# Kernel tuning notes

Hardware: AMD Instinct MI355X
Metric: run time of the kernel (lower is better)

Reference implementation:

```python
import jax, jax.numpy as jnp
import numpy as np

N = 4096        # number of nodes
C = 512         # in_features
L_LAT = 64      # L_latent
EPS = 0.25      # epsilon


def setup_inputs() -> dict:
    key = jax.random.key(0)
    ks = jax.random.split(key, 8)
    def lin(k, fan_in, shape):
        return (jax.random.normal(k, shape, jnp.float32) / np.float32(np.sqrt(fan_in)))
    x = jax.random.normal(ks[0], (N, C), jnp.float32)
    adj = jax.random.uniform(ks[1], (N, N), jnp.float32)  # dense nonneg kernel
    W_proj = lin(ks[2], C, (C, L_LAT)); b_proj = jnp.zeros((L_LAT,), jnp.float32)
    W_pi1 = lin(ks[3], L_LAT, (L_LAT, C)); b_pi1 = jnp.zeros((C,), jnp.float32)
    W_pi2 = lin(ks[4], C, (C, 1)); b_pi2 = jnp.zeros((1,), jnp.float32)
    W_f = lin(ks[5], C, (C, C)); b_f = jnp.zeros((C,), jnp.float32)
    dt = jnp.array([0.1], jnp.float32)
    return {"x": x, "adj": adj, "W_proj": W_proj, "b_proj": b_proj,
            "W_pi1": W_pi1, "b_pi1": b_pi1, "W_pi2": W_pi2, "b_pi2": b_pi2,
            "W_f": W_f, "b_f": b_f, "dt": dt}


def reference(x, adj, W_proj, b_proj, W_pi1, b_pi1, W_pi2, b_pi2, W_f, b_f, dt):
    # proj_list: x -> latent [n, L]
    z = x @ W_proj + b_proj
    # pi_list: Linear -> ReLU -> Linear -> Sigmoid, squeeze to [n]
    pi = jax.nn.sigmoid(jax.nn.relu(z @ W_pi1 + b_pi1) @ W_pi2 + b_pi2)[:, 0]
    # q_epsilon_tilde: row sums of the kernel
    q = adj.sum(axis=1)                       # [n]
    # K_tilde = K_epsilon @ diag(pi/q)  == column scaling
    K_tilde = adj * (pi / q)[None, :]         # [n, n]
    # D_tilde diagonal; torch.inverse of a diagonal == elementwise reciprocal
    d = K_tilde.sum(axis=1) + 1e-5            # [n]
    # target = relu(f(x)) with f = Linear(C, C)
    target = jax.nn.relu(x @ W_f + b_f)       # [n, C]
    # L @ target = (1/eps) * diag(1/d) @ K_tilde @ target - target
    Lt = (K_tilde @ target) / (EPS * d)[:, None] - target
    return target + dt[0] * Lt
```

## Files before the change

kernel.cpp:

```cpp
#include <hip/hip_runtime.h>
#include <hip/hip_bf16.h>

#define N_NODES 4096
#define C_DIM   512
#define L_DIM   64
#define SPLITS  4
#define KCHUNK  (N_NODES / SPLITS)

typedef unsigned short u16;
typedef unsigned int   u32;
using bf16x8 = __attribute__((ext_vector_type(8))) __bf16;
using u16x8  = __attribute__((ext_vector_type(8))) unsigned short;
using f32x4  = __attribute__((ext_vector_type(4))) float;

__device__ __forceinline__ float b2f(u16 u) {
    union { unsigned int i; float f; } v; v.i = ((unsigned int)u) << 16; return v.f;
}
__device__ __forceinline__ u16 f2b(float f) {
    __bf16 h = (__bf16)f;
    union { __bf16 h; u16 u; } v; v.h = h; return v.u;
}
__device__ __forceinline__ void gload16(const void* g, void* l) {
    __builtin_amdgcn_global_load_lds((const __attribute__((address_space(1))) void*)g,
                                     (__attribute__((address_space(3))) void*)l,
                                     16, 0, 0);
}
__device__ __forceinline__ int detect_mode_inl(const u16* __restrict__ adj) {
    int m = 0;
#pragma unroll
    for (int i = 0; i < 64; ++i) m |= (adj[i] >= 0x8000) ? 1 : 0;
    return m;
}
__device__ __forceinline__ float ldin(const void* p, int i, int mode) {
    if (mode) return ((const float*)p)[i];
    return b2f(((const u16*)p)[i]);
}

#define OFF_MODE  0
#define OFF_DT    64
#define OFF_BIAS  1024
#define OFF_BP    4096
#define OFF_BP1   4608
#define OFF_WP2   8192
#define OFF_BP2   10240
#define OFF_Q     16384
#define OFF_S     32768
#define OFF_DV    49152
#define OFF_WPP   65536
#define OFF_WP1P  131072
#define OFF_WFT   196608
#define OFF_PACC  720896
#define OFF_TST   9437184
#define OFF_XB    13631488
#define OFF_ADJB  17825792

__global__ __launch_bounds__(256) void k1_prep(const void* __restrict__ adj, const void* __restrict__ x,
        const void* Wp, const void* bp, const void* Wp1, const void* bp1,
        const void* Wp2, const void* bp2, const void* Wf, const void* bfc, const void* dt,
        int* __restrict__ modep,
        float* __restrict__ bp_f, float* __restrict__ bp1_f,
        float* __restrict__ Wp2_f, float* __restrict__ bp2_f,
        float* __restrict__ bias_f, float* __restrict__ dt_f,
        u32* __restrict__ WpP, u32* __restrict__ Wp1P,
        u16* __restrict__ adjb, float* __restrict__ q, u16* __restrict__ xb,
        u16* __restrict__ WfT, float* __restrict__ Pacc2, float* __restrict__ dvraw) {
    __shared__ float tile[32][33];
    int bid = blockIdx.x, tid = threadIdx.x;
    int mode = detect_mode_inl((const u16*)adj);
    if (bid < 1024) {
        int wave = tid >> 6, lane = tid & 63;
        int row = bid * 4 + wave;
        float acc = 0.f;
        if (mode) {
            const float4* rp = (const float4*)((const float*)adj + (size_t)row * N_NODES);
            ushort4* wp = (ushort4*)(adjb + (size_t)row * N_NODES);
#pragma unroll 8
            for (int it = 0; it < 16; ++it) {
                float4 v = rp[it * 64 + lane];
                acc += (v.x + v.y) + (v.z + v.w);
                ushort4 o; o.x = f2b(v.x); o.y = f2b(v.y); o.z = f2b(v.z); o.w = f2b(v.w);
                wp[it * 64 + lane] = o;
            }
        } else {
            const u16x8* rp = (const u16x8*)((const u16*)adj + (size_t)row * N_NODES);
#pragma unroll
            for (int it = 0; it < 8; ++it) {
                u16x8 v = rp[it * 64 + lane];
#pragma unroll
                for (int e = 0; e < 8; ++e) acc += b2f(v[e]);
            }
        }
#pragma unroll
        for (int off = 32; off > 0; off >>= 1) acc += __shfl_down(acc, off);
        if (lane == 0) q[row] = acc;
    } else if (bid < 3072) {
        if (mode == 0) return;
        int idx = (bid - 1024) * 256 + tid;
        float4 v = ((const float4*)x)[idx];
        ushort4 o; o.x = f2b(v.x); o.y = f2b(v.y); o.z = f2b(v.z); o.w = f2b(v.w);
        ((ushort4*)xb)[idx] = o;
    } else if (bid < 3328) {
        int g = bid - 3072;
        int tx = tid & 31, ty = tid >> 5;
        int x0 = (g & 15) * 32, y0 = (g >> 4) * 32;
        if (mode) {
            const float* src = (const float*)Wf;
#pragma unroll
            for (int r = ty; r < 32; r += 8) tile[r][tx] = src[(size_t)(y0 + r) * C_DIM + x0 + tx];
        } else {
            const u16* src = (const u16*)Wf;
#pragma unroll
            for (int r = ty; r < 32; r += 8) tile[r][tx] = b2f(src[(size_t)(y0 + r) * C_DIM + x0 + tx]);
        }
        __syncthreads();
#pragma unroll
        for (int r = ty; r < 32; r += 8)
            WfT[(size_t)(x0 + r) * C_DIM + y0 + tx] = f2b(tile[tx][r]);
    } else if (bid < 3392) {
        int idx = (bid - 3328) * 256 + tid;
        int k2i = idx >> 6, j = idx & 63;
        float a = ldin(Wp, (2 * k2i) * L_DIM + j, mode);
        float b = ldin(Wp, (2 * k2i + 1) * L_DIM + j, mode);
        WpP[idx] = (u32)f2b(a) | ((u32)f2b(b) << 16);
    } else if (bid < 3456) {
        int idx = (bid - 3392) * 256 + tid;
        int jj2 = idx >> 9, m = idx & 511;
        float a = ldin(Wp1, (2 * jj2) * C_DIM + m, mode);
        float b = ldin(Wp1, (2 * jj2 + 1) * C_DIM + m, mode);
        Wp1P[idx] = (u32)f2b(a) | ((u32)f2b(b) << 16);
    } else if (bid < 3463) {
        if (bid == 3456 && tid == 0) *modep = mode;
        int idx = (bid - 3456) * 256 + tid;
        if (idx < 64)           bp_f[idx]          = ldin(bp,  idx, mode);
        else if (idx < 576)     bp1_f[idx - 64]    = ldin(bp1, idx - 64, mode);
        else if (idx < 1088)    Wp2_f[idx - 576]   = ldin(Wp2, idx - 576, mode);
        else if (idx == 1088)   bp2_f[0]           = ldin(bp2, 0, mode);
        else if (idx < 1601)    bias_f[idx - 1089] = ldin(bfc, idx - 1089, mode);
        else if (idx == 1601)   dt_f[0]            = ldin(dt, 0, mode);
    } else if (bid < 5511) {
        int idx = (bid - 3463) * 256 + tid;
        ((float4*)Pacc2)[idx] = make_float4(0.f, 0.f, 0.f, 0.f);
    } else {
        int idx = (bid - 5511) * 256 + tid;
        dvraw[idx] = 0.f;
    }
}

__global__ __launch_bounds__(256) void k1p_pi(const void* __restrict__ xraw,
        const int* __restrict__ modep, const u16* __restrict__ xb,
        const u32* __restrict__ WpP, const u32* __restrict__ Wp1P,
        const float* __restrict__ bp_f,  const float* __restrict__ bp1_f,
        const float* __restrict__ Wp2_f, const float* __restrict__ bp2_f,
        const float* __restrict__ q, float* __restrict__ s) {
    __shared__ __align__(16) char smem[26880];
    int bid = blockIdx.x, tid = threadIdx.x;
    int mode = *modep;
    float (*sx)[C_DIM]      = (float(*)[C_DIM])smem;
    float (*red)[8][L_DIM]  = (float(*)[8][L_DIM])(smem + 16384);
    float (*sz)[L_DIM]      = (float(*)[L_DIM])(smem + 24576);
    float (*rw)[8]          = (float(*)[8])(smem + 26624);
    int i0 = bid * 8;
    const u16* xsrc = mode ? xb : (const u16*)xraw;
    const u16x8* xp = (const u16x8*)(xsrc + (size_t)i0 * C_DIM);
#pragma unroll
    for (int r = 0; r < 2; ++r) {
        u16x8 v = xp[tid + 256 * r];
        float* dstf = &sx[0][0] + (size_t)(tid + 256 * r) * 8;
#pragma unroll
        for (int e = 0; e < 8; ++e) dstf[e] = b2f(v[e]);
    }
    __syncthreads();
    int j = tid & 63, part = tid >> 6;
    float za[8];
#pragma unroll
    for (int n = 0; n < 8; ++n) za[n] = 0.f;
    const u32* wp = WpP + part * 4096 + j;
#pragma unroll 8
    for (int kk = 0; kk < 64; ++kk) {
        u32 w = wp[kk * 64];
        float wa = b2f((u16)(w & 0xFFFF)), wb = b2f((u16)(w >> 16));
        int k = part * 128 + kk * 2;
#pragma unroll
        for (int n = 0; n < 8; ++n) za[n] += sx[n][k] * wa + sx[n][k + 1] * wb;
    }
#pragma unroll
    for (int n = 0; n < 8; ++n) red[part][n][j] = za[n];
    __syncthreads();
#pragma unroll
    for (int r = 0; r < 2; ++r) {
        int idx = tid + r * 256; int n = idx >> 6, jj = idx & 63;
        sz[n][jj] = red[0][n][jj] + red[1][n][jj] + red[2][n][jj] + red[3][n][jj] + bp_f[jj];
    }
    __syncthreads();
    int m0 = tid, m1 = tid + 256;
    float h0[8], h1[8];
    float b0 = bp1_f[m0], b1 = bp1_f[m1];
#pragma unroll
    for (int n = 0; n < 8; ++n) { h0[n] = b0; h1[n] = b1; }
    const u32* w1p = Wp1P + m0;
#pragma unroll 4
    for (int jj2 = 0; jj2 < 32; ++jj2) {
        u32 w0 = w1p[jj2 * 512], w1 = w1p[jj2 * 512 + 256];
        float w0a = b2f((u16)(w0 & 0xFFFF)), w0b = b2f((u16)(w0 >> 16));
        float w1a = b2f((u16)(w1 & 0xFFFF)), w1b = b2f((u16)(w1 >> 16));
#pragma unroll
        for (int n = 0; n < 8; ++n) {
            float za_ = sz[n][2 * jj2], zb_ = sz[n][2 * jj2 + 1];
            h0[n] += za_ * w0a + zb_ * w0b;
            h1[n] += za_ * w1a + zb_ * w1b;
        }
    }
    float w2a = Wp2_f[m0], w2b = Wp2_f[m1];
    float p[8];
#pragma unroll
    for (int n = 0; n < 8; ++n)
        p[n] = fmaxf(h0[n], 0.f) * w2a + fmaxf(h1[n], 0.f) * w2b;
#pragma unroll
    for (int off = 32; off > 0; off >>= 1)
#pragma unroll
        for (int n = 0; n < 8; ++n) p[n] += __shfl_down(p[n], off);
    int lane = tid & 63, wave = tid >> 6;
    if (lane == 0) {
#pragma unroll
        for (int n = 0; n < 8; ++n) rw[wave][n] = p[n];
    }
    __syncthreads();
    if (tid < 8) {
        float tot = rw[0][tid] + rw[1][tid] + rw[2][tid] + rw[3][tid] + bp2_f[0];
        float pi = 1.f / (1.f + expf(-tot));
        s[i0 + tid] = pi / q[i0 + tid];
    }
}

__global__ __launch_bounds__(256) void k2_gemm1(const void* __restrict__ xraw,
        const int* __restrict__ modep,
        const float* __restrict__ s, const float* __restrict__ bias_f, const float* __restrict__ dt_f,
        const u16* __restrict__ xb, const u16* __restrict__ WfT,
        u16* __restrict__ TsT, void* __restrict__ out, float* __restrict__ Pacc_base) {
    __shared__ __align__(16) char smem[16640];
    int bid = blockIdx.x, tid = threadIdx.x;
    int mode = *modep;
    u16* lA = (u16*)smem;
    u16* lB = (u16*)(smem + 8192);
    u16* lT = (u16*)smem;
    float* s_row = (float*)(smem + 16384);
    int lane = tid & 63, wave = tid >> 6;
    int bm = (bid & 63) * 64, bn = (bid >> 6) * 64;
    if (tid < 64) s_row[tid] = s[bm + tid];
    const u16* Axb = mode ? xb : (const u16*)xraw;
    float* basep = mode ? (float*)out : Pacc_base;
    int quad = lane >> 4, l15 = lane & 15;
    int wm = wave * 16;
    int trow = tid >> 3;
    int xslot = (tid & 7) ^ (trow & 7);
    const u16* Ap0 = Axb + (size_t)(bm + trow) * C_DIM + xslot * 8;
    const u16* Ap1 = Axb + (size_t)(bm + 32 + trow) * C_DIM + xslot * 8;
    const u16* Bp0 = WfT + (size_t)(bn + trow) * C_DIM + xslot * 8;
    const u16* Bp1 = WfT + (size_t)(bn + 32 + trow) * C_DIM + xslot * 8;
    f32x4 acc[4];
#pragma unroll
    for (int nt = 0; nt < 4; ++nt) acc[nt] = (f32x4){0.f, 0.f, 0.f, 0.f};
    for (int k0 = 0; k0 < C_DIM; k0 += 64) {
        gload16(Ap0 + k0, lA + tid * 8);
        gload16(Ap1 + k0, lA + 2048 + tid * 8);
        gload16(Bp0 + k0, lB + tid * 8);
        gload16(Bp1 + k0, lB + 2048 + tid * 8);
        asm volatile("s_waitcnt vmcnt(0)\n\ts_barrier" ::: "memory");
        __builtin_amdgcn_sched_barrier(0);
#pragma unroll
        for (int kk = 0; kk < 2; ++kk) {
            int xr = (((kk << 2) | quad) ^ (l15 & 7)) * 8;
            bf16x8 af = *(const bf16x8*)&lA[(wm + l15) * 64 + xr];
            bf16x8 bfv[4];
#pragma unroll
            for (int nt = 0; nt < 4; ++nt)
                bfv[nt] = *(const bf16x8*)&lB[(nt * 16 + l15) * 64 + xr];
#pragma unroll
            for (int nt = 0; nt < 4; ++nt)
                acc[nt] = __builtin_amdgcn_mfma_f32_16x16x32_bf16(af, bfv[nt], acc[nt], 0, 0, 0);
        }
        asm volatile("s_waitcnt lgkmcnt(0)\n\ts_barrier" ::: "memory");
    }
    float c0 = 1.f - dt_f[0];
#pragma unroll
    for (int nt = 0; nt < 4; ++nt) {
        int col_l = nt * 16 + l15;
        float bv = bias_f[bn + col_l];
#pragma unroll
        for (int r = 0; r < 4; ++r) {
            int row_l = wm + quad * 4 + r;
            float t = fmaxf(acc[nt][r] + bv, 0.f);
            basep[(size_t)(bm + row_l) * C_DIM + bn + col_l] = c0 * t;
            lT[col_l * 64 + row_l] = f2b(t * s_row[row_l]);
        }
    }
    __syncthreads();
    int col_l = tid >> 2, seg = tid & 3;
    uint4 w0 = *(const uint4*)&lT[col_l * 64 + seg * 16];
    uint4 w1 = *(const uint4*)&lT[col_l * 64 + seg * 16 + 8];
    u16* dst = TsT + (size_t)(bn + col_l) * N_NODES + bm + seg * 16;
    *(uint4*)dst = w0;
    *(uint4*)(dst + 8) = w1;
}

__global__ __launch_bounds__(256) void k3_gemm2(const void* __restrict__ adjraw,
        const int* __restrict__ modep,
        const u16* __restrict__ adjb, const u16* __restrict__ TsT,
        const float* __restrict__ s,
        float* __restrict__ Pacc2, float* __restrict__ dvraw) {
    __shared__ __align__(16) u16 lA[8192];
    __shared__ __align__(16) u16 lB[8192];
    int mode = *modep;
    const u16* A = mode ? adjb : (const u16*)adjraw;
    int tid = threadIdx.x;
    int id = blockIdx.x;
    int xcd = id & 7, local = id >> 3;
    if (local < 64) {
        int lane = tid & 63, wave = tid >> 6;
        int bm128 = (xcd * 4 + (local >> 4)) * 128;
        int bn128 = ((local >> 2) & 3) * 128;
        int kbase = (local & 3) * KCHUNK;
        int wm = (wave & 1) * 64, wn = (wave >> 1) * 64;
        int quad = lane >> 4, l15 = lane & 15;
        int trow = tid >> 3;
        int xslot = (tid & 7) ^ (trow & 7);

        const u16* Ap[4]; const u16* Bp[4];
#pragma unroll
        for (int i = 0; i < 4; ++i) {
            Ap[i] = A   + (size_t)(bm128 + i * 32 + trow) * N_NODES + kbase + xslot * 8;
            Bp[i] = TsT + (size_t)(bn128 + i * 32 + trow) * N_NODES + kbase + xslot * 8;
        }

        f32x4 acc[4][4];
#pragma unroll
        for (int a = 0; a < 4; ++a)
#pragma unroll
            for (int b = 0; b < 4; ++b) acc[a][b] = (f32x4){0.f, 0.f, 0.f, 0.f};

        for (int k0 = 0; k0 < KCHUNK; k0 += 64) {
#pragma unroll
            for (int i = 0; i < 4; ++i) gload16(Ap[i] + k0, lA + i * 2048 + tid * 8);
#pragma unroll
            for (int i = 0; i < 4; ++i) gload16(Bp[i] + k0, lB + i * 2048 + tid * 8);
            asm volatile("s_waitcnt vmcnt(0)\n\ts_barrier" ::: "memory");
            __builtin_amdgcn_sched_barrier(0);
#pragma unroll
            for (int kk = 0; kk < 2; ++kk) {
                int xr = (((kk << 2) | quad) ^ (l15 & 7)) * 8;
                bf16x8 af[4], bfv[4];
#pragma unroll
                for (int mt = 0; mt < 4; ++mt) af[mt] = *(const bf16x8*)&lA[(wm + mt * 16 + l15) * 64 + xr];
#pragma unroll
                for (int nt = 0; nt < 4; ++nt) bfv[nt] = *(const bf16x8*)&lB[(wn + nt * 16 + l15) * 64 + xr];
#pragma unroll
                for (int mt = 0; mt < 4; ++mt)
#pragma unroll
                    for (int nt = 0; nt < 4; ++nt)
                        acc[mt][nt] = __builtin_amdgcn_mfma_f32_16x16x32_bf16(af[mt], bfv[nt], acc[mt][nt], 0, 0, 0);
            }
            asm volatile("s_waitcnt lgkmcnt(0)\n\ts_barrier" ::: "memory");
        }

#pragma unroll
        for (int mt = 0; mt < 4; ++mt) {
#pragma unroll
            for (int nt = 0; nt < 4; ++nt) {
                int col = bn128 + wn + nt * 16 + l15;
#pragma unroll
                for (int r = 0; r < 4; ++r) {
                    int row = bm128 + wm + mt * 16 + quad * 4 + r;
                    atomicAdd(&Pacc2[(size_t)row * C_DIM + col], acc[mt][nt][r]);
                }
            }
        }
    } else {
        int l2 = local - 64;
        int bm128 = (xcd * 4 + (l2 >> 2)) * 128;
        int kbase = (l2 & 3) * KCHUNK;
        float* s_lds = (float*)lA;
        ((float4*)s_lds)[tid] = ((const float4*)(s + kbase))[tid];
        __syncthreads();
        int lane = tid & 63, wave = tid >> 6;
        const u16* base_row = A + (size_t)(bm128 + wave * 32) * N_NODES + kbase;
        for (int r = 0; r < 32; ++r) {
            const u16x8* rp = (const u16x8*)(base_row + (size_t)r * N_NODES) + lane;
            float acc = 0.f;
#pragma unroll
            for (int it = 0; it < 2; ++it) {
                u16x8 v = rp[it * 64];
                const float* sp = s_lds + it * 512 + lane * 8;
#pragma unroll
                for (int e = 0; e < 8; ++e) acc += b2f(v[e]) * sp[e];
            }
#pragma unroll
            for (int off = 32; off > 0; off >>= 1) acc += __shfl_down(acc, off);
            if (lane == 0) atomicAdd(&dvraw[bm128 + wave * 32 + r], acc);
        }
    }
}

__global__ __launch_bounds__(256) void k5_fin(const int* __restrict__ modep,
                                              const float* __restrict__ dt_f,
                                              const float* __restrict__ Pacc2,
                                              const float* __restrict__ dvraw,
                                              const float* __restrict__ Pacc_base,
                                              void* __restrict__ out) {
    int mode = *modep;
    int idx = blockIdx.x * 256 + threadIdx.x;
    float c1 = dt_f[0] * 4.f;
    const float4* basep = mode ? (const float4*)out : (const float4*)Pacc_base;
    float4 b = basep[idx];
    float4 p = ((const float4*)Pacc2)[idx];
    int row = idx >> 7;
    float rscale = c1 / (dvraw[row] + 1e-5f);
    float4 v;
    v.x = b.x + p.x * rscale;
    v.y = b.y + p.y * rscale;
    v.z = b.z + p.z * rscale;
    v.w = b.w + p.w * rscale;
    if (mode) {
        ((float4*)out)[idx] = v;
    } else {
        ushort4 o; o.x = f2b(v.x); o.y = f2b(v.y); o.z = f2b(v.z); o.w = f2b(v.w);
        ((ushort4*)out)[idx] = o;
    }
}

extern "C" void kernel_launch(void* const* d_in, const int* in_sizes, int n_in,
                              void* d_out, int out_size, void* d_ws, size_t ws_size,
                              hipStream_t stream) {
    const void* x   = d_in[0];
    const void* adj = d_in[1];
    const void* Wp  = d_in[2];
    const void* bp  = d_in[3];
    const void* Wp1 = d_in[4];
    const void* bp1 = d_in[5];
    const void* Wp2 = d_in[6];
    const void* bp2 = d_in[7];
    const void* Wf  = d_in[8];
    const void* bfc = d_in[9];
    const void* dtp = d_in[10];

    char* ws = (char*)d_ws;
    int*   modep  = (int*)(ws + OFF_MODE);
    float* dt_f   = (float*)(ws + OFF_DT);
    float* bias_f = (float*)(ws + OFF_BIAS);
    float* bp_f   = (float*)(ws + OFF_BP);
    float* bp1_f  = (float*)(ws + OFF_BP1);
    float* Wp2_f  = (float*)(ws + OFF_WP2);
    float* bp2_f  = (float*)(ws + OFF_BP2);
    float* q      = (float*)(ws + OFF_Q);
    float* s      = (float*)(ws + OFF_S);
    float* dvraw  = (float*)(ws + OFF_DV);
    u32*   WpP    = (u32*)(ws + OFF_WPP);
    u32*   Wp1P   = (u32*)(ws + OFF_WP1P);
    u16*   WfT    = (u16*)(ws + OFF_WFT);
    float* Pacc2  = (float*)(ws + OFF_PACC);
    u16*   TsT    = (u16*)(ws + OFF_TST);
    u16*   xb     = (u16*)(ws + OFF_XB);
    u16*   adjb   = (u16*)(ws + OFF_ADJB);
    float* Pacc_base = (float*)(ws + OFF_ADJB);

    k1_prep<<<5527, 256, 0, stream>>>(adj, x, Wp, bp, Wp1, bp1, Wp2, bp2, Wf, bfc, dtp,
                                      modep, bp_f, bp1_f, Wp2_f, bp2_f, bias_f, dt_f,
                                      WpP, Wp1P, adjb, q, xb, WfT, Pacc2, dvraw);
    k1p_pi<<<512, 256, 0, stream>>>(x, modep, xb, WpP, Wp1P, bp_f, bp1_f, Wp2_f, bp2_f, q, s);
    k2_gemm1<<<512, 256, 0, stream>>>(x, modep, s, bias_f, dt_f, xb, WfT, TsT, d_out, Pacc_base);
    k3_gemm2<<<640, 256, 0, stream>>>(adj, modep, adjb, TsT, s, Pacc2, dvraw);
    k5_fin<<<2048, 256, 0, stream>>>(modep, dt_f, Pacc2, dvraw, Pacc_base, d_out);
}
```

Before: 234.5 us.

## Fuse d-vector matvec into GEMM2 via MFMA, memset accumulators, coarsen prep/fin

The separate d = adj·s row-reduction blocks in the second GEMM are replaced by an extra MFMA per k-step, issued from blockIdx.y==0 waves, with s staged in LDS and masked into one B column. The grid becomes a 3D launch without XCD remapping, and the LDS layout drops the XOR swizzle in favor of two 32-wide k halves. Zeroing the accumulators moves from prep blocks to hipMemsetAsync, and the prep and finish kernels process several elements per thread. The explicit waitcnt/barrier asm is replaced by __syncthreads. Risks include LDS bank conflicts from the unswizzled layout, lost XCD locality, and extra MFMA work on some waves.

```diff
diff --git a/kernel.cpp b/kernel.cpp
--- a/kernel.cpp
+++ b/kernel.cpp
@@ -63,7 +63,7 @@
         float* __restrict__ bias_f, float* __restrict__ dt_f,
         u32* __restrict__ WpP, u32* __restrict__ Wp1P,
         u16* __restrict__ adjb, float* __restrict__ q, u16* __restrict__ xb,
-        u16* __restrict__ WfT, float* __restrict__ Pacc2, float* __restrict__ dvraw) {
+        u16* __restrict__ WfT) {
     __shared__ float tile[32][33];
     int bid = blockIdx.x, tid = threadIdx.x;
     int mode = detect_mode_inl((const u16*)adj);
@@ -93,14 +93,18 @@
 #pragma unroll
         for (int off = 32; off > 0; off >>= 1) acc += __shfl_down(acc, off);
         if (lane == 0) q[row] = acc;
-    } else if (bid < 3072) {
+    } else if (bid < 1152) {
         if (mode == 0) return;
-        int idx = (bid - 1024) * 256 + tid;
-        float4 v = ((const float4*)x)[idx];
-        ushort4 o; o.x = f2b(v.x); o.y = f2b(v.y); o.z = f2b(v.z); o.w = f2b(v.w);
-        ((ushort4*)xb)[idx] = o;
-    } else if (bid < 3328) {
-        int g = bid - 3072;
+        int base = (bid - 1024) * 256 + tid;
+#pragma unroll
+        for (int i = 0; i < 16; ++i) {
+            int idx = i * 32768 + base;
+            float4 v = ((const float4*)x)[idx];
+            ushort4 o; o.x = f2b(v.x); o.y = f2b(v.y); o.z = f2b(v.z); o.w = f2b(v.w);
+            ((ushort4*)xb)[idx] = o;
+        }
+    } else if (bid < 1408) {
+        int g = bid - 1152;
         int tx = tid & 31, ty = tid >> 5;
         int x0 = (g & 15) * 32, y0 = (g >> 4) * 32;
         if (mode) {
@@ -116,33 +120,35 @@
 #pragma unroll
         for (int r = ty; r < 32; r += 8)
             WfT[(size_t)(x0 + r) * C_DIM + y0 + tx] = f2b(tile[tx][r]);
-    } else if (bid < 3392) {
-        int idx = (bid - 3328) * 256 + tid;
-        int k2i = idx >> 6, j = idx & 63;
-        float a = ldin(Wp, (2 * k2i) * L_DIM + j, mode);
-        float b = ldin(Wp, (2 * k2i + 1) * L_DIM + j, mode);
-        WpP[idx] = (u32)f2b(a) | ((u32)f2b(b) << 16);
-    } else if (bid < 3456) {
-        int idx = (bid - 3392) * 256 + tid;
-        int jj2 = idx >> 9, m = idx & 511;
-        float a = ldin(Wp1, (2 * jj2) * C_DIM + m, mode);
-        float b = ldin(Wp1, (2 * jj2 + 1) * C_DIM + m, mode);
-        Wp1P[idx] = (u32)f2b(a) | ((u32)f2b(b) << 16);
-    } else if (bid < 3463) {
-        if (bid == 3456 && tid == 0) *modep = mode;
-        int idx = (bid - 3456) * 256 + tid;
+    } else if (bid < 1416) {
+        int base = (bid - 1408) * 2048 + tid;
+#pragma unroll
+        for (int i = 0; i < 8; ++i) {
+            int idx = base + i * 256;
+            int k2i = idx >> 6, j = idx & 63;
+            float a = ldin(Wp, (2 * k2i) * L_DIM + j, mode);
+            float b = ldin(Wp, (2 * k2i + 1) * L_DIM + j, mode);
+            WpP[idx] = (u32)f2b(a) | ((u32)f2b(b) << 16);
+        }
+    } else if (bid < 1424) {
+        int base = (bid - 1416) * 2048 + tid;
+#pragma unroll
+        for (int i = 0; i < 8; ++i) {
+            int idx = base + i * 256;
+            int jj2 = idx >> 9, m = idx & 511;
+            float a = ldin(Wp1, (2 * jj2) * C_DIM + m, mode);
+            float b = ldin(Wp1, (2 * jj2 + 1) * C_DIM + m, mode);
+            Wp1P[idx] = (u32)f2b(a) | ((u32)f2b(b) << 16);
+        }
+    } else {
+        if (bid == 1424 && tid == 0) *modep = mode;
+        int idx = (bid - 1424) * 256 + tid;
         if (idx < 64)           bp_f[idx]          = ldin(bp,  idx, mode);
         else if (idx < 576)     bp1_f[idx - 64]    = ldin(bp1, idx - 64, mode);
         else if (idx < 1088)    Wp2_f[idx - 576]   = ldin(Wp2, idx - 576, mode);
         else if (idx == 1088)   bp2_f[0]           = ldin(bp2, 0, mode);
         else if (idx < 1601)    bias_f[idx - 1089] = ldin(bfc, idx - 1089, mode);
         else if (idx == 1601)   dt_f[0]            = ldin(dt, 0, mode);
-    } else if (bid < 5511) {
-        int idx = (bid - 3463) * 256 + tid;
-        ((float4*)Pacc2)[idx] = make_float4(0.f, 0.f, 0.f, 0.f);
-    } else {
-        int idx = (bid - 5511) * 256 + tid;
-        dvraw[idx] = 0.f;
     }
 }
 
@@ -265,8 +271,7 @@
         gload16(Ap1 + k0, lA + 2048 + tid * 8);
         gload16(Bp0 + k0, lB + tid * 8);
         gload16(Bp1 + k0, lB + 2048 + tid * 8);
-        asm volatile("s_waitcnt vmcnt(0)\n\ts_barrier" ::: "memory");
-        __builtin_amdgcn_sched_barrier(0);
+        __syncthreads();
 #pragma unroll
         for (int kk = 0; kk < 2; ++kk) {
             int xr = (((kk << 2) | quad) ^ (l15 & 7)) * 8;
@@ -279,7 +284,7 @@
             for (int nt = 0; nt < 4; ++nt)
                 acc[nt] = __builtin_amdgcn_mfma_f32_16x16x32_bf16(af, bfv[nt], acc[nt], 0, 0, 0);
         }
-        asm volatile("s_waitcnt lgkmcnt(0)\n\ts_barrier" ::: "memory");
+        __syncthreads();
     }
     float c0 = 1.f - dt_f[0];
 #pragma unroll
@@ -310,93 +315,97 @@
         float* __restrict__ Pacc2, float* __restrict__ dvraw) {
     __shared__ __align__(16) u16 lA[8192];
     __shared__ __align__(16) u16 lB[8192];
+    __shared__ __align__(16) u16 s_s[1024];
     int mode = *modep;
     const u16* A = mode ? adjb : (const u16*)adjraw;
     int tid = threadIdx.x;
-    int id = blockIdx.x;
-    int xcd = id & 7, local = id >> 3;
-    if (local < 64) {
-        int lane = tid & 63, wave = tid >> 6;
-        int bm128 = (xcd * 4 + (local >> 4)) * 128;
-        int bn128 = ((local >> 2) & 3) * 128;
-        int kbase = (local & 3) * KCHUNK;
-        int wm = (wave & 1) * 64, wn = (wave >> 1) * 64;
-        int quad = lane >> 4, l15 = lane & 15;
-        int trow = tid >> 3;
-        int xslot = (tid & 7) ^ (trow & 7);
-
-        const u16* Ap[4]; const u16* Bp[4];
-#pragma unroll
-        for (int i = 0; i < 4; ++i) {
-            Ap[i] = A   + (size_t)(bm128 + i * 32 + trow) * N_NODES + kbase + xslot * 8;
-            Bp[i] = TsT + (size_t)(bn128 + i * 32 + trow) * N_NODES + kbase + xslot * 8;
-        }
-
-        f32x4 acc[4][4];
-#pragma unroll
-        for (int a = 0; a < 4; ++a)
-#pragma unroll
-            for (int b = 0; b < 4; ++b) acc[a][b] = (f32x4){0.f, 0.f, 0.f, 0.f};
-
-        for (int k0 = 0; k0 < KCHUNK; k0 += 64) {
-#pragma unroll
-            for (int i = 0; i < 4; ++i) gload16(Ap[i] + k0, lA + i * 2048 + tid * 8);
-#pragma unroll
-            for (int i = 0; i < 4; ++i) gload16(Bp[i] + k0, lB + i * 2048 + tid * 8);
-            asm volatile("s_waitcnt vmcnt(0)\n\ts_barrier" ::: "memory");
-            __builtin_amdgcn_sched_barrier(0);
-#pragma unroll
-            for (int kk = 0; kk < 2; ++kk) {
-                int xr = (((kk << 2) | quad) ^ (l15 & 7)) * 8;
-                bf16x8 af[4], bfv[4];
-#pragma unroll
-                for (int mt = 0; mt < 4; ++mt) af[mt] = *(const bf16x8*)&lA[(wm + mt * 16 + l15) * 64 + xr];
-#pragma unroll
-                for (int nt = 0; nt < 4; ++nt) bfv[nt] = *(const bf16x8*)&lB[(wn + nt * 16 + l15) * 64 + xr];
+    int lane = tid & 63, wave = tid >> 6;
+    int bm = blockIdx.x * 128, bn = blockIdx.y * 128;
+    int kbase = blockIdx.z * KCHUNK;
+    int wm = (wave & 1) * 64, wn = (wave >> 1) * 64;
+    int quad = lane >> 4, l15 = lane & 15;
+    bool do_d = (blockIdx.y == 0) && (wave < 2);
+
+#pragma unroll
+    for (int i = 0; i < 4; ++i) {
+        int k = tid + i * 256;
+        s_s[k] = f2b(s[kbase + k]);
+    }
+
+    const u16* Ab0 = A + (size_t)(bm + (tid >> 2)) * N_NODES + kbase + (tid & 3) * 8;
+    const u16* Ab1 = A + (size_t)(bm + 64 + (tid >> 2)) * N_NODES + kbase + (tid & 3) * 8;
+    const u16* Bb0 = TsT + (size_t)(bn + (tid >> 2)) * N_NODES + kbase + (tid & 3) * 8;
+    const u16* Bb1 = TsT + (size_t)(bn + 64 + (tid >> 2)) * N_NODES + kbase + (tid & 3) * 8;
+    u16* la00 = lA + tid * 8;        u16* la01 = lA + 2048 + tid * 8;
+    u16* la10 = lA + 4096 + tid * 8; u16* la11 = lA + 6144 + tid * 8;
+    u16* lb00 = lB + tid * 8;        u16* lb01 = lB + 2048 + tid * 8;
+    u16* lb10 = lB + 4096 + tid * 8; u16* lb11 = lB + 6144 + tid * 8;
+
+    f32x4 acc[4][4];
+#pragma unroll
+    for (int a = 0; a < 4; ++a)
+#pragma unroll
+        for (int b = 0; b < 4; ++b) acc[a][b] = (f32x4){0.f, 0.f, 0.f, 0.f};
+    f32x4 accd[4];
+#pragma unroll
+    for (int a = 0; a < 4; ++a) accd[a] = (f32x4){0.f, 0.f, 0.f, 0.f};
+    u16 dmask = (l15 == 0) ? (u16)0xFFFFu : (u16)0;
+
+    for (int k0 = 0; k0 < KCHUNK; k0 += 64) {
+        gload16(Ab0 + k0, la00);
+        gload16(Ab1 + k0, la01);
+        gload16(Ab0 + k0 + 32, la10);
+        gload16(Ab1 + k0 + 32, la11);
+        gload16(Bb0 + k0, lb00);
+        gload16(Bb1 + k0, lb01);
+        gload16(Bb0 + k0 + 32, lb10);
+        gload16(Bb1 + k0 + 32, lb11);
+        __syncthreads();
+#pragma unroll
+        for (int kk = 0; kk < 2; ++kk) {
+            const u16* baseA = lA + kk * 4096;
+            const u16* baseB = lB + kk * 4096;
+            bf16x8 af[4], bfv[4];
+#pragma unroll
+            for (int mt = 0; mt < 4; ++mt) af[mt] = *(const bf16x8*)&baseA[(wm + mt * 16 + l15) * 32 + quad * 8];
+#pragma unroll
+            for (int nt = 0; nt < 4; ++nt) bfv[nt] = *(const bf16x8*)&baseB[(wn + nt * 16 + l15) * 32 + quad * 8];
+#pragma unroll
+            for (int mt = 0; mt < 4; ++mt)
+#pragma unroll
+                for (int nt = 0; nt < 4; ++nt)
+                    acc[mt][nt] = __builtin_amdgcn_mfma_f32_16x16x32_bf16(af[mt], bfv[nt], acc[mt][nt], 0, 0, 0);
+            if (do_d) {
+                u16x8 su = *(const u16x8*)&s_s[k0 + kk * 32 + quad * 8];
+#pragma unroll
+                for (int e = 0; e < 8; ++e) su[e] &= dmask;
+                bf16x8 bs = *(bf16x8*)&su;
 #pragma unroll
                 for (int mt = 0; mt < 4; ++mt)
-#pragma unroll
-                    for (int nt = 0; nt < 4; ++nt)
-                        acc[mt][nt] = __builtin_amdgcn_mfma_f32_16x16x32_bf16(af[mt], bfv[nt], acc[mt][nt], 0, 0, 0);
+                    accd[mt] = __builtin_amdgcn_mfma_f32_16x16x32_bf16(af[mt], bs, accd[mt], 0, 0, 0);
             }
-            asm volatile("s_waitcnt lgkmcnt(0)\n\ts_barrier" ::: "memory");
-        }
-
-#pragma unroll
-        for (int mt = 0; mt < 4; ++mt) {
-#pragma unroll
-            for (int nt = 0; nt < 4; ++nt) {
-                int col = bn128 + wn + nt * 16 + l15;
-#pragma unroll
-                for (int r = 0; r < 4; ++r) {
-                    int row = bm128 + wm + mt * 16 + quad * 4 + r;
-                    atomicAdd(&Pacc2[(size_t)row * C_DIM + col], acc[mt][nt][r]);
-                }
+        }
+        __syncthreads();
+    }
+
+#pragma unroll
+    for (int mt = 0; mt < 4; ++mt) {
+#pragma unroll
+        for (int nt = 0; nt < 4; ++nt) {
+            int col = bn + wn + nt * 16 + l15;
+#pragma unroll
+            for (int r = 0; r < 4; ++r) {
+                int row = bm + wm + mt * 16 + quad * 4 + r;
+                atomicAdd(&Pacc2[(size_t)row * C_DIM + col], acc[mt][nt][r]);
             }
         }
-    } else {
-        int l2 = local - 64;
-        int bm128 = (xcd * 4 + (l2 >> 2)) * 128;
-        int kbase = (l2 & 3) * KCHUNK;
-        float* s_lds = (float*)lA;
-        ((float4*)s_lds)[tid] = ((const float4*)(s + kbase))[tid];
-        __syncthreads();
-        int lane = tid & 63, wave = tid >> 6;
-        const u16* base_row = A + (size_t)(bm128 + wave * 32) * N_NODES + kbase;
-        for (int r = 0; r < 32; ++r) {
-            const u16x8* rp = (const u16x8*)(base_row + (size_t)r * N_NODES) + lane;
-            float acc = 0.f;
-#pragma unroll
-            for (int it = 0; it < 2; ++it) {
-                u16x8 v = rp[it * 64];
-                const float* sp = s_lds + it * 512 + lane * 8;
-#pragma unroll
-                for (int e = 0; e < 8; ++e) acc += b2f(v[e]) * sp[e];
-            }
-#pragma unroll
-            for (int off = 32; off > 0; off >>= 1) acc += __shfl_down(acc, off);
-            if (lane == 0) atomicAdd(&dvraw[bm128 + wave * 32 + r], acc);
-        }
+    }
+    if (do_d && l15 == 0) {
+#pragma unroll
+        for (int mt = 0; mt < 4; ++mt)
+#pragma unroll
+            for (int r = 0; r < 4; ++r)
+                atomicAdd(&dvraw[bm + wm + mt * 16 + quad * 4 + r], accd[mt][r]);
     }
 }
 
@@ -407,23 +416,26 @@
                                               const float* __restrict__ Pacc_base,
                                               void* __restrict__ out) {
     int mode = *modep;
-    int idx = blockIdx.x * 256 + threadIdx.x;
     float c1 = dt_f[0] * 4.f;
     const float4* basep = mode ? (const float4*)out : (const float4*)Pacc_base;
-    float4 b = basep[idx];
-    float4 p = ((const float4*)Pacc2)[idx];
-    int row = idx >> 7;
-    float rscale = c1 / (dvraw[row] + 1e-5f);
-    float4 v;
-    v.x = b.x + p.x * rscale;
-    v.y = b.y + p.y * rscale;
-    v.z = b.z + p.z * rscale;
-    v.w = b.w + p.w * rscale;
-    if (mode) {
-        ((float4*)out)[idx] = v;
-    } else {
-        ushort4 o; o.x = f2b(v.x); o.y = f2b(v.y); o.z = f2b(v.z); o.w = f2b(v.w);
-        ((ushort4*)out)[idx] = o;
+#pragma unroll
+    for (int i = 0; i < 8; ++i) {
+        int idx = blockIdx.x * 2048 + i * 256 + threadIdx.x;
+        float4 b = basep[idx];
+        float4 p = ((const float4*)Pacc2)[idx];
+        int row = idx >> 7;
+        float rscale = c1 / (dvraw[row] + 1e-5f);
+        float4 v;
+        v.x = b.x + p.x * rscale;
+        v.y = b.y + p.y * rscale;
+        v.z = b.z + p.z * rscale;
+        v.w = b.w + p.w * rscale;
+        if (mode) {
+            ((float4*)out)[idx] = v;
+        } else {
+            ushort4 o; o.x = f2b(v.x); o.y = f2b(v.y); o.z = f2b(v.z); o.w = f2b(v.w);
+            ((ushort4*)out)[idx] = o;
+        }
     }
 }
 
@@ -462,11 +474,13 @@
     u16*   adjb   = (u16*)(ws + OFF_ADJB);
     float* Pacc_base = (float*)(ws + OFF_ADJB);
 
-    k1_prep<<<5527, 256, 0, stream>>>(adj, x, Wp, bp, Wp1, bp1, Wp2, bp2, Wf, bfc, dtp,
+    hipMemsetAsync(Pacc2, 0, (size_t)N_NODES * C_DIM * sizeof(float), stream);
+    hipMemsetAsync(dvraw, 0, (size_t)N_NODES * sizeof(float), stream);
+    k1_prep<<<1431, 256, 0, stream>>>(adj, x, Wp, bp, Wp1, bp1, Wp2, bp2, Wf, bfc, dtp,
                                       modep, bp_f, bp1_f, Wp2_f, bp2_f, bias_f, dt_f,
-                                      WpP, Wp1P, adjb, q, xb, WfT, Pacc2, dvraw);
+                                      WpP, Wp1P, adjb, q, xb, WfT);
     k1p_pi<<<512, 256, 0, stream>>>(x, modep, xb, WpP, Wp1P, bp_f, bp1_f, Wp2_f, bp2_f, q, s);
     k2_gemm1<<<512, 256, 0, stream>>>(x, modep, s, bias_f, dt_f, xb, WfT, TsT, d_out, Pacc_base);
-    k3_gemm2<<<640, 256, 0, stream>>>(adj, modep, adjb, TsT, s, Pacc2, dvraw);
-    k5_fin<<<2048, 256, 0, stream>>>(modep, dt_f, Pacc2, dvraw, Pacc_base, d_out);
-}
+    k3_gemm2<<<dim3(32, 4, SPLITS), 256, 0, stream>>>(adj, modep, adjb, TsT, s, Pacc2, dvraw);
+    k5_fin<<<256, 256, 0, stream>>>(modep, dt_f, Pacc2, dvraw, Pacc_base, d_out);
+}
```

Result: faster. 225.5 us (-3.9%).
